# Optimization experiments

Hardware: AMD Instinct MI355X
Metric: run time of the kernel (lower is better)

Reference implementation:

```python
import jax, jax.numpy as jnp
import numpy as np

B, T, D, H = 8, 2048, 1024, 1024

def setup_inputs() -> dict:
    key = jax.random.key(0)
    k1, k2, k3, k4 = jax.random.split(key, 4)
    scale = 1.0 / np.sqrt(D)
    return {
        "x": jax.random.normal(k1, (B, T, D), dtype=jnp.float32),
        "Wq": jax.random.normal(k2, (D, H), dtype=jnp.float32) * scale,
        "Wk": jax.random.normal(k3, (D, H), dtype=jnp.float32) * scale,
        "Wv": jax.random.normal(k4, (D, H), dtype=jnp.float32) * scale,
    }

def reference(x, Wq, Wk, Wv):
    # Single-head causal self-attention (dropout in eval mode = identity)
    q = jnp.einsum('btd,dh->bth', x, Wq)
    k = jnp.einsum('btd,dh->bth', x, Wk)
    v = jnp.einsum('btd,dh->bth', x, Wv)
    inv_sqrt_h = 1.0 / jnp.sqrt(jnp.asarray(q.shape[-1], q.dtype))
    scores = jnp.einsum('bqh,bkh->bqk', q, k) * inv_sqrt_h  # [B, T, T]
    Tq = scores.shape[-1]
    causal = jnp.tril(jnp.ones((Tq, Tq), dtype=bool))
    scores = jnp.where(causal, scores, jnp.asarray(-jnp.inf, scores.dtype))
    weights = jax.nn.softmax(scores, axis=-1)
    return jnp.einsum('bqk,bkh->bqh', weights, v)
```

## Files before the change

### kernel.cpp

```cpp
#include <hip/hip_runtime.h>

#define Bn 8
#define Tn 2048
#define Dn 1024
#define Hn 1024
#define Mn (Bn * Tn)

typedef __attribute__((ext_vector_type(8))) short bf16x8;
typedef __attribute__((ext_vector_type(4))) short short4v;
typedef __attribute__((ext_vector_type(4))) float f32x4;

__device__ __forceinline__ unsigned short f2bf(float f) {
  union { float f; unsigned int u; } v; v.f = f;
  unsigned int u = v.u;
  u += 0x7FFFu + ((u >> 16) & 1u);
  return (unsigned short)(u >> 16);
}
__device__ __forceinline__ float bf2f(unsigned short h) {
  union { unsigned int u; float f; } v; v.u = ((unsigned int)h) << 16;
  return v.f;
}

__device__ __forceinline__ void gload_lds16(const unsigned short* g, unsigned short* l) {
  __builtin_amdgcn_global_load_lds((const __attribute__((address_space(1))) void*)g,
                                   (__attribute__((address_space(3))) void*)l, 16, 0, 0);
}

__device__ __forceinline__ void stage128x32(const unsigned short* gbase, size_t row_stride,
                                            unsigned short* lds, int wave, int lane) {
#pragma unroll
  for (int c = 0; c < 2; ++c) {
    const unsigned short* g =
        gbase + (size_t)(wave * 32 + c * 16 + (lane >> 2)) * row_stride + (lane & 3) * 8;
    gload_lds16(g, lds + (wave * 32 + c * 16) * 32);
  }
}

__device__ __forceinline__ void stage128x64(const unsigned short* gbase, size_t row_stride,
                                            unsigned short* lds0, unsigned short* lds1,
                                            int wave, int lane) {
  stage128x32(gbase, row_stride, lds0, wave, lane);
  stage128x32(gbase + 32, row_stride, lds1, wave, lane);
}

__global__ __launch_bounds__(256) void k_convert(const float* __restrict__ in,
                                                 unsigned short* __restrict__ out, int n4) {
  int idx = blockIdx.x * 256 + threadIdx.x;
  if (idx >= n4) return;
  float4 v = ((const float4*)in)[idx];
  short4v o;
  o.x = (short)f2bf(v.x); o.y = (short)f2bf(v.y);
  o.z = (short)f2bf(v.z); o.w = (short)f2bf(v.w);
  *(short4v*)(out + (size_t)idx * 4) = o;
}

__global__ __launch_bounds__(256) void k_cvt_w_t(const float* __restrict__ W,
                                                 unsigned short* __restrict__ Wt) {
  const int n0 = blockIdx.x * 64, k0 = blockIdx.y * 64;
  __shared__ unsigned short lT[64 * 65];
  const int tid = threadIdx.x;
#pragma unroll
  for (int p = 0; p < 2; ++p) {
    int o = tid + p * 256;
    int r = o >> 3, c = (o & 7) * 8;
    const float* src = W + (size_t)(k0 + r) * Hn + n0 + c;
    float4 v0 = *(const float4*)src;
    float4 v1 = *(const float4*)(src + 4);
    unsigned short* d = &lT[r * 65 + c];
    d[0] = f2bf(v0.x); d[1] = f2bf(v0.y); d[2] = f2bf(v0.z); d[3] = f2bf(v0.w);
    d[4] = f2bf(v1.x); d[5] = f2bf(v1.y); d[6] = f2bf(v1.z); d[7] = f2bf(v1.w);
  }
  __syncthreads();
#pragma unroll
  for (int p = 0; p < 2; ++p) {
    int o = tid + p * 256;
    int r2 = o >> 3, c2 = (o & 7) * 8;
    bf16x8 v;
#pragma unroll
    for (int s = 0; s < 8; ++s) v[s] = (short)lT[(c2 + s) * 65 + r2];
    *(bf16x8*)(Wt + (size_t)(n0 + r2) * Dn + k0 + c2) = v;
  }
}

__global__ __launch_bounds__(256) void gemm_qkv(const unsigned short* __restrict__ A,
                                                const unsigned short* __restrict__ Wt3,
                                                unsigned short* __restrict__ Q,
                                                unsigned short* __restrict__ Kb,
                                                unsigned short* __restrict__ Vt) {
  const int f = blockIdx.x;
  const int c = f & 7;
  const int q = f >> 3;
  const int nn = q % 24;
  const int w = nn >> 3;
  const int n0 = (nn & 7) * 128;
  const int m0 = ((q / 24) * 8 + c) * 128;
  const unsigned short* B = Wt3 + (size_t)w * Hn * Dn;
  __shared__ unsigned short lA[2][128 * 32];
  __shared__ unsigned short lB[2][128 * 32];
  const int tid = threadIdx.x;
  const int lane = tid & 63, wave = tid >> 6;
  const int wr = (wave >> 1) * 64, wc = (wave & 1) * 64;
  const int quad = lane >> 4, l16 = lane & 15;

  f32x4 acc[4][4];
#pragma unroll
  for (int i = 0; i < 4; ++i)
#pragma unroll
    for (int j = 0; j < 4; ++j) acc[i][j] = (f32x4){0.f, 0.f, 0.f, 0.f};

  for (int kt = 0; kt < Dn / 64; ++kt) {
    stage128x64(A + (size_t)m0 * Dn + kt * 64, Dn, lA[0], lA[1], wave, lane);
    stage128x64(B + (size_t)n0 * Dn + kt * 64, Dn, lB[0], lB[1], wave, lane);
    __syncthreads();
#pragma unroll
    for (int s = 0; s < 2; ++s) {
      bf16x8 af[4], bfr[4];
#pragma unroll
      for (int i = 0; i < 4; ++i) af[i] = *(const bf16x8*)&lA[s][(wr + i * 16 + l16) * 32 + quad * 8];
#pragma unroll
      for (int j = 0; j < 4; ++j) bfr[j] = *(const bf16x8*)&lB[s][(wc + j * 16 + l16) * 32 + quad * 8];
#pragma unroll
      for (int i = 0; i < 4; ++i)
#pragma unroll
        for (int j = 0; j < 4; ++j)
          acc[i][j] = __builtin_amdgcn_mfma_f32_16x16x32_bf16(af[i], bfr[j], acc[i][j], 0, 0, 0);
    }
    __syncthreads();
  }
  if (w != 2) {
    unsigned short* C = (w == 0) ? Q : Kb;
#pragma unroll
    for (int i = 0; i < 4; ++i)
#pragma unroll
      for (int j = 0; j < 4; ++j)
#pragma unroll
        for (int r = 0; r < 4; ++r) {
          int row = m0 + wr + i * 16 + quad * 4 + r;
          int col = n0 + wc + j * 16 + l16;
          C[(size_t)row * Hn + col] = f2bf(acc[i][j][r]);
        }
  } else {
    const int bb = m0 >> 11;
    const int tb = m0 & 2047;
#pragma unroll
    for (int i = 0; i < 4; ++i)
#pragma unroll
      for (int j = 0; j < 4; ++j) {
        int t0 = tb + wr + i * 16 + quad * 4;
        int h = n0 + wc + j * 16 + l16;
        short4v o;
        o.x = (short)f2bf(acc[i][j][0]);
        o.y = (short)f2bf(acc[i][j][1]);
        o.z = (short)f2bf(acc[i][j][2]);
        o.w = (short)f2bf(acc[i][j][3]);
        *(short4v*)(Vt + ((size_t)bb * Hn + h) * Tn + t0) = o;
      }
  }
}

__global__ __launch_bounds__(256) void gemm_scores(const unsigned short* __restrict__ Q,
                                                   const unsigned short* __restrict__ K,
                                                   unsigned short* __restrict__ S) {
  const int f = blockIdx.x;
  const int b = f & 7;
  const int q = f >> 3;
  const int rt = 15 - (q & 15);
  const int ct = q >> 4;
  if (ct > rt) return;
  const int j0 = ct * 128, i0 = rt * 128;
  const unsigned short* Qb = Q + (size_t)b * Tn * Hn;
  const unsigned short* Kb = K + (size_t)b * Tn * Hn;
  unsigned short* Sb = S + (size_t)b * Tn * Tn;
  __shared__ unsigned short lA[2][128 * 32];
  __shared__ unsigned short lB[2][128 * 32];
  const int tid = threadIdx.x;
  const int lane = tid & 63, wave = tid >> 6;
  const int wr = (wave >> 1) * 64, wc = (wave & 1) * 64;
  const int quad = lane >> 4, l16 = lane & 15;

  f32x4 acc[4][4];
#pragma unroll
  for (int i = 0; i < 4; ++i)
#pragma unroll
    for (int j = 0; j < 4; ++j) acc[i][j] = (f32x4){0.f, 0.f, 0.f, 0.f};

  for (int kt = 0; kt < Hn / 64; ++kt) {
    stage128x64(Qb + (size_t)i0 * Hn + kt * 64, Hn, lA[0], lA[1], wave, lane);
    stage128x64(Kb + (size_t)j0 * Hn + kt * 64, Hn, lB[0], lB[1], wave, lane);
    __syncthreads();
#pragma unroll
    for (int s = 0; s < 2; ++s) {
      bf16x8 af[4], bfr[4];
#pragma unroll
      for (int i = 0; i < 4; ++i) af[i] = *(const bf16x8*)&lA[s][(wr + i * 16 + l16) * 32 + quad * 8];
#pragma unroll
      for (int j = 0; j < 4; ++j) bfr[j] = *(const bf16x8*)&lB[s][(wc + j * 16 + l16) * 32 + quad * 8];
#pragma unroll
      for (int i = 0; i < 4; ++i)
#pragma unroll
        for (int j = 0; j < 4; ++j)
          acc[i][j] = __builtin_amdgcn_mfma_f32_16x16x32_bf16(af[i], bfr[j], acc[i][j], 0, 0, 0);
    }
    __syncthreads();
  }
#pragma unroll
  for (int i = 0; i < 4; ++i)
#pragma unroll
    for (int j = 0; j < 4; ++j)
#pragma unroll
      for (int r = 0; r < 4; ++r) {
        int row = i0 + wr + i * 16 + quad * 4 + r;
        int col = j0 + wc + j * 16 + l16;
        float e = (col <= row) ? __expf(acc[i][j][r] * 0.03125f) : 0.f;
        Sb[(size_t)row * Tn + col] = f2bf(e);
      }
}

__global__ __launch_bounds__(256) void k_rowsum(const unsigned short* __restrict__ S,
                                                float* __restrict__ l) {
  const int b = blockIdx.y;
  const int i = blockIdx.x * 4 + (threadIdx.x >> 6);
  const int lane = threadIdx.x & 63;
  const unsigned short* row = S + ((size_t)b * Tn + i) * (size_t)Tn;
  const int npad = ((i >> 7) + 1) << 7;
  float s = 0.f;
  for (int j0 = 0; j0 < npad; j0 += 512) {
    int j = j0 + lane * 8;
    if (j < npad) {
      bf16x8 v = *(const bf16x8*)(row + j);
#pragma unroll
      for (int t = 0; t < 8; ++t) s += bf2f((unsigned short)v[t]);
    }
  }
#pragma unroll
  for (int off = 32; off > 0; off >>= 1) s += __shfl_down(s, off);
  if (lane == 0) l[(size_t)b * Tn + i] = s;
}

__global__ __launch_bounds__(256) void gemm_out(const unsigned short* __restrict__ P,
                                                const unsigned short* __restrict__ Vt,
                                                const float* __restrict__ lbuf,
                                                float* __restrict__ O) {
  const int f = blockIdx.x;
  const int b = f & 7;
  const int q = f >> 3;
  const int n0 = (q & 7) * 128;
  const int rt = 15 - (q >> 3);
  const int i0 = rt * 128;
  const int nkt = (rt + 1) * 2;
  const unsigned short* Pb = P + (size_t)b * Tn * Tn;
  const unsigned short* Vb = Vt + (size_t)b * Tn * Hn;
  __shared__ unsigned short lA[2][128 * 32];
  __shared__ unsigned short lB[2][128 * 32];
  const int tid = threadIdx.x;
  const int lane = tid & 63, wave = tid >> 6;
  const int wr = (wave >> 1) * 64, wc = (wave & 1) * 64;
  const int quad = lane >> 4, l16 = lane & 15;

  f32x4 acc[4][4];
#pragma unroll
  for (int i = 0; i < 4; ++i)
#pragma unroll
    for (int j = 0; j < 4; ++j) acc[i][j] = (f32x4){0.f, 0.f, 0.f, 0.f};

  for (int kt = 0; kt < nkt; ++kt) {
    stage128x64(Pb + (size_t)i0 * Tn + kt * 64, Tn, lA[0], lA[1], wave, lane);
    stage128x64(Vb + (size_t)n0 * Tn + kt * 64, Tn, lB[0], lB[1], wave, lane);
    __syncthreads();
#pragma unroll
    for (int s = 0; s < 2; ++s) {
      bf16x8 af[4], bfr[4];
#pragma unroll
      for (int i = 0; i < 4; ++i) af[i] = *(const bf16x8*)&lA[s][(wr + i * 16 + l16) * 32 + quad * 8];
#pragma unroll
      for (int j = 0; j < 4; ++j) bfr[j] = *(const bf16x8*)&lB[s][(wc + j * 16 + l16) * 32 + quad * 8];
#pragma unroll
      for (int i = 0; i < 4; ++i)
#pragma unroll
        for (int j = 0; j < 4; ++j)
          acc[i][j] = __builtin_amdgcn_mfma_f32_16x16x32_bf16(af[i], bfr[j], acc[i][j], 0, 0, 0);
    }
    __syncthreads();
  }
  float linv[4][4];
#pragma unroll
  for (int i = 0; i < 4; ++i)
#pragma unroll
    for (int r = 0; r < 4; ++r)
      linv[i][r] = 1.f / lbuf[(size_t)b * Tn + (i0 + wr + i * 16 + quad * 4 + r)];
#pragma unroll
  for (int i = 0; i < 4; ++i)
#pragma unroll
    for (int j = 0; j < 4; ++j)
#pragma unroll
      for (int r = 0; r < 4; ++r) {
        int row = i0 + wr + i * 16 + quad * 4 + r;
        int col = n0 + wc + j * 16 + l16;
        O[((size_t)b * Tn + row) * Hn + col] = acc[i][j][r] * linv[i][r];
      }
}

extern "C" void kernel_launch(void* const* d_in, const int* in_sizes, int n_in,
                              void* d_out, int out_size, void* d_ws, size_t ws_size,
                              hipStream_t stream) {
  const float* x  = (const float*)d_in[0];
  const float* Wq = (const float*)d_in[1];
  const float* Wk = (const float*)d_in[2];
  const float* Wv = (const float*)d_in[3];
  float* out = (float*)d_out;

  char* ws = (char*)d_ws;
  const size_t MiB = 1024 * 1024;
  unsigned short* Wt3 = (unsigned short*)(ws + 0 * MiB);
  unsigned short* xb  = (unsigned short*)(ws + 6 * MiB);
  unsigned short* Qb  = (unsigned short*)(ws + 38 * MiB);
  unsigned short* Kb  = (unsigned short*)(ws + 70 * MiB);
  unsigned short* Vt  = (unsigned short*)(ws + 102 * MiB);
  unsigned short* S   = (unsigned short*)(ws + 134 * MiB);
  float*          lrow = (float*)(ws + 6 * MiB);

  {
    int n4 = (Mn * Dn) / 4;
    k_convert<<<dim3(n4 / 256), 256, 0, stream>>>(x, xb, n4);
  }
  {
    dim3 g(Hn / 64, Dn / 64);
    k_cvt_w_t<<<g, 256, 0, stream>>>(Wq, Wt3);
    k_cvt_w_t<<<g, 256, 0, stream>>>(Wk, Wt3 + (size_t)Hn * Dn);
    k_cvt_w_t<<<g, 256, 0, stream>>>(Wv, Wt3 + (size_t)2 * Hn * Dn);
  }
  {
    gemm_qkv<<<dim3(3072), 256, 0, stream>>>(xb, Wt3, Qb, Kb, Vt);
  }
  {
    gemm_scores<<<dim3(2048), 256, 0, stream>>>(Qb, Kb, S);
  }
  {
    k_rowsum<<<dim3(Tn / 4, Bn), 256, 0, stream>>>(S, lrow);
  }
  {
    gemm_out<<<dim3(1024), 256, 0, stream>>>(S, Vt, lrow, out);
  }
}
```

Measured before the change: 368.8 us.

## Switch GEMMs to 32x32x16 MFMA with XOR-swizzled LDS staging

All three GEMM kernels (QKV projection, scores, output) move from 16x16x32 bf16 MFMA tiles to 32x32x16 tiles, so each wave holds four 16-wide accumulators instead of sixteen 4-wide ones. Global-to-LDS staging now XOR-swizzles the 16-byte column chunk by row, which is meant to cut LDS bank conflicts on fragment reads. The three weight-transpose launches are merged into one launch over a z grid dimension. The epilogues are rewritten for the 32x32 accumulator layout, including a vectorized float4 load of the row sums in the output kernel.

```diff
diff --git a/kernel.cpp b/kernel.cpp
--- a/kernel.cpp
+++ b/kernel.cpp
@@ -8,7 +8,7 @@
 
 typedef __attribute__((ext_vector_type(8))) short bf16x8;
 typedef __attribute__((ext_vector_type(4))) short short4v;
-typedef __attribute__((ext_vector_type(4))) float f32x4;
+typedef __attribute__((ext_vector_type(16))) float f32x16;
 
 __device__ __forceinline__ unsigned short f2bf(float f) {
   union { float f; unsigned int u; } v; v.f = f;
@@ -26,21 +26,42 @@
                                    (__attribute__((address_space(3))) void*)l, 16, 0, 0);
 }
 
-__device__ __forceinline__ void stage128x32(const unsigned short* gbase, size_t row_stride,
-                                            unsigned short* lds, int wave, int lane) {
+__device__ __forceinline__ void stage128x32s(const unsigned short* gbase, size_t row_stride,
+                                             unsigned short* lds, int wave, int lane) {
 #pragma unroll
   for (int c = 0; c < 2; ++c) {
-    const unsigned short* g =
-        gbase + (size_t)(wave * 32 + c * 16 + (lane >> 2)) * row_stride + (lane & 3) * 8;
+    int rl = c * 16 + (lane >> 2);
+    int pos = (lane & 3) ^ (rl & 3);
+    const unsigned short* g = gbase + (size_t)(wave * 32 + rl) * row_stride + pos * 8;
     gload_lds16(g, lds + (wave * 32 + c * 16) * 32);
   }
 }
-
-__device__ __forceinline__ void stage128x64(const unsigned short* gbase, size_t row_stride,
-                                            unsigned short* lds0, unsigned short* lds1,
-                                            int wave, int lane) {
-  stage128x32(gbase, row_stride, lds0, wave, lane);
-  stage128x32(gbase + 32, row_stride, lds1, wave, lane);
+__device__ __forceinline__ void stage128x64s(const unsigned short* gbase, size_t row_stride,
+                                             unsigned short* lds0, unsigned short* lds1,
+                                             int wave, int lane) {
+  stage128x32s(gbase, row_stride, lds0, wave, lane);
+  stage128x32s(gbase + 32, row_stride, lds1, wave, lane);
+}
+
+__device__ __forceinline__ void mma_bk32(const unsigned short* lA, const unsigned short* lB,
+                                         int wr, int wc, int l32, int half,
+                                         f32x16 acc[2][2]) {
+#pragma unroll
+  for (int kk = 0; kk < 2; ++kk) {
+    const int pos = (kk * 2 + half) ^ (l32 & 3);
+    bf16x8 af[2], bfr[2];
+#pragma unroll
+    for (int m = 0; m < 2; ++m)
+      af[m] = *(const bf16x8*)&lA[(wr + m * 32 + l32) * 32 + pos * 8];
+#pragma unroll
+    for (int n = 0; n < 2; ++n)
+      bfr[n] = *(const bf16x8*)&lB[(wc + n * 32 + l32) * 32 + pos * 8];
+#pragma unroll
+    for (int m = 0; m < 2; ++m)
+#pragma unroll
+      for (int n = 0; n < 2; ++n)
+        acc[m][n] = __builtin_amdgcn_mfma_f32_32x32x16_bf16(af[m], bfr[n], acc[m][n], 0, 0, 0);
+  }
 }
 
 __global__ __launch_bounds__(256) void k_convert(const float* __restrict__ in,
@@ -54,9 +75,13 @@
   *(short4v*)(out + (size_t)idx * 4) = o;
 }
 
-__global__ __launch_bounds__(256) void k_cvt_w_t(const float* __restrict__ W,
-                                                 unsigned short* __restrict__ Wt) {
-  const int n0 = blockIdx.x * 64, k0 = blockIdx.y * 64;
+__global__ __launch_bounds__(256) void k_cvt_w_t(const float* __restrict__ W0,
+                                                 const float* __restrict__ W1,
+                                                 const float* __restrict__ W2,
+                                                 unsigned short* __restrict__ Wt3) {
+  const int n0 = blockIdx.x * 64, k0 = blockIdx.y * 64, w = blockIdx.z;
+  const float* W = (w == 0) ? W0 : (w == 1) ? W1 : W2;
+  unsigned short* Wt = Wt3 + (size_t)w * Hn * Dn;
   __shared__ unsigned short lT[64 * 65];
   const int tid = threadIdx.x;
 #pragma unroll
@@ -100,60 +125,55 @@
   const int tid = threadIdx.x;
   const int lane = tid & 63, wave = tid >> 6;
   const int wr = (wave >> 1) * 64, wc = (wave & 1) * 64;
-  const int quad = lane >> 4, l16 = lane & 15;
-
-  f32x4 acc[4][4];
-#pragma unroll
-  for (int i = 0; i < 4; ++i)
-#pragma unroll
-    for (int j = 0; j < 4; ++j) acc[i][j] = (f32x4){0.f, 0.f, 0.f, 0.f};
+  const int l32 = lane & 31, half = lane >> 5;
+
+  f32x16 acc[2][2];
+#pragma unroll
+  for (int m = 0; m < 2; ++m)
+#pragma unroll
+    for (int n = 0; n < 2; ++n) acc[m][n] = (f32x16)(0.f);
 
   for (int kt = 0; kt < Dn / 64; ++kt) {
-    stage128x64(A + (size_t)m0 * Dn + kt * 64, Dn, lA[0], lA[1], wave, lane);
-    stage128x64(B + (size_t)n0 * Dn + kt * 64, Dn, lB[0], lB[1], wave, lane);
-    __syncthreads();
-#pragma unroll
-    for (int s = 0; s < 2; ++s) {
-      bf16x8 af[4], bfr[4];
-#pragma unroll
-      for (int i = 0; i < 4; ++i) af[i] = *(const bf16x8*)&lA[s][(wr + i * 16 + l16) * 32 + quad * 8];
-#pragma unroll
-      for (int j = 0; j < 4; ++j) bfr[j] = *(const bf16x8*)&lB[s][(wc + j * 16 + l16) * 32 + quad * 8];
-#pragma unroll
-      for (int i = 0; i < 4; ++i)
-#pragma unroll
-        for (int j = 0; j < 4; ++j)
-          acc[i][j] = __builtin_amdgcn_mfma_f32_16x16x32_bf16(af[i], bfr[j], acc[i][j], 0, 0, 0);
-    }
+    stage128x64s(A + (size_t)m0 * Dn + kt * 64, Dn, lA[0], lA[1], wave, lane);
+    stage128x64s(B + (size_t)n0 * Dn + kt * 64, Dn, lB[0], lB[1], wave, lane);
+    __syncthreads();
+    mma_bk32(lA[0], lB[0], wr, wc, l32, half, acc);
+    mma_bk32(lA[1], lB[1], wr, wc, l32, half, acc);
     __syncthreads();
   }
   if (w != 2) {
     unsigned short* C = (w == 0) ? Q : Kb;
 #pragma unroll
-    for (int i = 0; i < 4; ++i)
-#pragma unroll
-      for (int j = 0; j < 4; ++j)
-#pragma unroll
-        for (int r = 0; r < 4; ++r) {
-          int row = m0 + wr + i * 16 + quad * 4 + r;
-          int col = n0 + wc + j * 16 + l16;
-          C[(size_t)row * Hn + col] = f2bf(acc[i][j][r]);
+    for (int m = 0; m < 2; ++m)
+#pragma unroll
+      for (int n = 0; n < 2; ++n) {
+        int col = n0 + wc + n * 32 + l32;
+#pragma unroll
+        for (int qd = 0; qd < 4; ++qd) {
+          int rb = m0 + wr + m * 32 + 8 * qd + 4 * half;
+#pragma unroll
+          for (int rr = 0; rr < 4; ++rr)
+            C[(size_t)(rb + rr) * Hn + col] = f2bf(acc[m][n][qd * 4 + rr]);
         }
+      }
   } else {
     const int bb = m0 >> 11;
     const int tb = m0 & 2047;
 #pragma unroll
-    for (int i = 0; i < 4; ++i)
-#pragma unroll
-      for (int j = 0; j < 4; ++j) {
-        int t0 = tb + wr + i * 16 + quad * 4;
-        int h = n0 + wc + j * 16 + l16;
-        short4v o;
-        o.x = (short)f2bf(acc[i][j][0]);
-        o.y = (short)f2bf(acc[i][j][1]);
-        o.z = (short)f2bf(acc[i][j][2]);
-        o.w = (short)f2bf(acc[i][j][3]);
-        *(short4v*)(Vt + ((size_t)bb * Hn + h) * Tn + t0) = o;
+    for (int m = 0; m < 2; ++m)
+#pragma unroll
+      for (int n = 0; n < 2; ++n) {
+        int h = n0 + wc + n * 32 + l32;
+#pragma unroll
+        for (int qd = 0; qd < 4; ++qd) {
+          int t0 = tb + wr + m * 32 + 8 * qd + 4 * half;
+          short4v o;
+          o.x = (short)f2bf(acc[m][n][qd * 4 + 0]);
+          o.y = (short)f2bf(acc[m][n][qd * 4 + 1]);
+          o.z = (short)f2bf(acc[m][n][qd * 4 + 2]);
+          o.w = (short)f2bf(acc[m][n][qd * 4 + 3]);
+          *(short4v*)(Vt + ((size_t)bb * Hn + h) * Tn + t0) = o;
+        }
       }
   }
 }
@@ -169,51 +189,45 @@
   if (ct > rt) return;
   const int j0 = ct * 128, i0 = rt * 128;
   const unsigned short* Qb = Q + (size_t)b * Tn * Hn;
-  const unsigned short* Kb = K + (size_t)b * Tn * Hn;
+  const unsigned short* Kp = K + (size_t)b * Tn * Hn;
   unsigned short* Sb = S + (size_t)b * Tn * Tn;
   __shared__ unsigned short lA[2][128 * 32];
   __shared__ unsigned short lB[2][128 * 32];
   const int tid = threadIdx.x;
   const int lane = tid & 63, wave = tid >> 6;
   const int wr = (wave >> 1) * 64, wc = (wave & 1) * 64;
-  const int quad = lane >> 4, l16 = lane & 15;
-
-  f32x4 acc[4][4];
-#pragma unroll
-  for (int i = 0; i < 4; ++i)
-#pragma unroll
-    for (int j = 0; j < 4; ++j) acc[i][j] = (f32x4){0.f, 0.f, 0.f, 0.f};
+  const int l32 = lane & 31, half = lane >> 5;
+
+  f32x16 acc[2][2];
+#pragma unroll
+  for (int m = 0; m < 2; ++m)
+#pragma unroll
+    for (int n = 0; n < 2; ++n) acc[m][n] = (f32x16)(0.f);
 
   for (int kt = 0; kt < Hn / 64; ++kt) {
-    stage128x64(Qb + (size_t)i0 * Hn + kt * 64, Hn, lA[0], lA[1], wave, lane);
-    stage128x64(Kb + (size_t)j0 * Hn + kt * 64, Hn, lB[0], lB[1], wave, lane);
-    __syncthreads();
-#pragma unroll
-    for (int s = 0; s < 2; ++s) {
-      bf16x8 af[4], bfr[4];
-#pragma unroll
-      for (int i = 0; i < 4; ++i) af[i] = *(const bf16x8*)&lA[s][(wr + i * 16 + l16) * 32 + quad * 8];
-#pragma unroll
-      for (int j = 0; j < 4; ++j) bfr[j] = *(const bf16x8*)&lB[s][(wc + j * 16 + l16) * 32 + quad * 8];
-#pragma unroll
-      for (int i = 0; i < 4; ++i)
-#pragma unroll
-        for (int j = 0; j < 4; ++j)
-          acc[i][j] = __builtin_amdgcn_mfma_f32_16x16x32_bf16(af[i], bfr[j], acc[i][j], 0, 0, 0);
+    stage128x64s(Qb + (size_t)i0 * Hn + kt * 64, Hn, lA[0], lA[1], wave, lane);
+    stage128x64s(Kp + (size_t)j0 * Hn + kt * 64, Hn, lB[0], lB[1], wave, lane);
+    __syncthreads();
+    mma_bk32(lA[0], lB[0], wr, wc, l32, half, acc);
+    mma_bk32(lA[1], lB[1], wr, wc, l32, half, acc);
+    __syncthreads();
+  }
+#pragma unroll
+  for (int m = 0; m < 2; ++m)
+#pragma unroll
+    for (int n = 0; n < 2; ++n) {
+      int col = j0 + wc + n * 32 + l32;
+#pragma unroll
+      for (int qd = 0; qd < 4; ++qd) {
+        int rb = i0 + wr + m * 32 + 8 * qd + 4 * half;
+#pragma unroll
+        for (int rr = 0; rr < 4; ++rr) {
+          int row = rb + rr;
+          float e = (col <= row) ? __expf(acc[m][n][qd * 4 + rr] * 0.03125f) : 0.f;
+          Sb[(size_t)row * Tn + col] = f2bf(e);
+        }
+      }
     }
-    __syncthreads();
-  }
-#pragma unroll
-  for (int i = 0; i < 4; ++i)
-#pragma unroll
-    for (int j = 0; j < 4; ++j)
-#pragma unroll
-      for (int r = 0; r < 4; ++r) {
-        int row = i0 + wr + i * 16 + quad * 4 + r;
-        int col = j0 + wc + j * 16 + l16;
-        float e = (col <= row) ? __expf(acc[i][j][r] * 0.03125f) : 0.f;
-        Sb[(size_t)row * Tn + col] = f2bf(e);
-      }
 }
 
 __global__ __launch_bounds__(256) void k_rowsum(const unsigned short* __restrict__ S,
@@ -255,49 +269,38 @@
   const int tid = threadIdx.x;
   const int lane = tid & 63, wave = tid >> 6;
   const int wr = (wave >> 1) * 64, wc = (wave & 1) * 64;
-  const int quad = lane >> 4, l16 = lane & 15;
-
-  f32x4 acc[4][4];
-#pragma unroll
-  for (int i = 0; i < 4; ++i)
-#pragma unroll
-    for (int j = 0; j < 4; ++j) acc[i][j] = (f32x4){0.f, 0.f, 0.f, 0.f};
+  const int l32 = lane & 31, half = lane >> 5;
+
+  f32x16 acc[2][2];
+#pragma unroll
+  for (int m = 0; m < 2; ++m)
+#pragma unroll
+    for (int n = 0; n < 2; ++n) acc[m][n] = (f32x16)(0.f);
 
   for (int kt = 0; kt < nkt; ++kt) {
-    stage128x64(Pb + (size_t)i0 * Tn + kt * 64, Tn, lA[0], lA[1], wave, lane);
-    stage128x64(Vb + (size_t)n0 * Tn + kt * 64, Tn, lB[0], lB[1], wave, lane);
-    __syncthreads();
-#pragma unroll
-    for (int s = 0; s < 2; ++s) {
-      bf16x8 af[4], bfr[4];
-#pragma unroll
-      for (int i = 0; i < 4; ++i) af[i] = *(const bf16x8*)&lA[s][(wr + i * 16 + l16) * 32 + quad * 8];
-#pragma unroll
-      for (int j = 0; j < 4; ++j) bfr[j] = *(const bf16x8*)&lB[s][(wc + j * 16 + l16) * 32 + quad * 8];
-#pragma unroll
-      for (int i = 0; i < 4; ++i)
-#pragma unroll
-        for (int j = 0; j < 4; ++j)
-          acc[i][j] = __builtin_amdgcn_mfma_f32_16x16x32_bf16(af[i], bfr[j], acc[i][j], 0, 0, 0);
+    stage128x64s(Pb + (size_t)i0 * Tn + kt * 64, Tn, lA[0], lA[1], wave, lane);
+    stage128x64s(Vb + (size_t)n0 * Tn + kt * 64, Tn, lB[0], lB[1], wave, lane);
+    __syncthreads();
+    mma_bk32(lA[0], lB[0], wr, wc, l32, half, acc);
+    mma_bk32(lA[1], lB[1], wr, wc, l32, half, acc);
+    __syncthreads();
+  }
+#pragma unroll
+  for (int m = 0; m < 2; ++m)
+#pragma unroll
+    for (int n = 0; n < 2; ++n) {
+      int col = n0 + wc + n * 32 + l32;
+#pragma unroll
+      for (int qd = 0; qd < 4; ++qd) {
+        int rb = i0 + wr + m * 32 + 8 * qd + 4 * half;
+        float4 lv = *(const float4*)&lbuf[(size_t)b * Tn + rb];
+#pragma unroll
+        for (int rr = 0; rr < 4; ++rr) {
+          float inv = 1.f / ((&lv.x)[rr]);
+          O[((size_t)b * Tn + rb + rr) * Hn + col] = acc[m][n][qd * 4 + rr] * inv;
+        }
+      }
     }
-    __syncthreads();
-  }
-  float linv[4][4];
-#pragma unroll
-  for (int i = 0; i < 4; ++i)
-#pragma unroll
-    for (int r = 0; r < 4; ++r)
-      linv[i][r] = 1.f / lbuf[(size_t)b * Tn + (i0 + wr + i * 16 + quad * 4 + r)];
-#pragma unroll
-  for (int i = 0; i < 4; ++i)
-#pragma unroll
-    for (int j = 0; j < 4; ++j)
-#pragma unroll
-      for (int r = 0; r < 4; ++r) {
-        int row = i0 + wr + i * 16 + quad * 4 + r;
-        int col = n0 + wc + j * 16 + l16;
-        O[((size_t)b * Tn + row) * Hn + col] = acc[i][j][r] * linv[i][r];
-      }
 }
 
 extern "C" void kernel_launch(void* const* d_in, const int* in_sizes, int n_in,
@@ -324,10 +327,8 @@
     k_convert<<<dim3(n4 / 256), 256, 0, stream>>>(x, xb, n4);
   }
   {
-    dim3 g(Hn / 64, Dn / 64);
-    k_cvt_w_t<<<g, 256, 0, stream>>>(Wq, Wt3);
-    k_cvt_w_t<<<g, 256, 0, stream>>>(Wk, Wt3 + (size_t)Hn * Dn);
-    k_cvt_w_t<<<g, 256, 0, stream>>>(Wv, Wt3 + (size_t)2 * Hn * Dn);
+    dim3 g(Hn / 64, Dn / 64, 3);
+    k_cvt_w_t<<<g, 256, 0, stream>>>(Wq, Wk, Wv, Wt3);
   }
   {
     gemm_qkv<<<dim3(3072), 256, 0, stream>>>(xb, Wt3, Qb, Kb, Vt);
```

New measurement: 367.8 us. About the same (-0.3%).
